# Optimization experiments

Hardware: AMD Instinct MI355X
Metric: run time of the kernel (lower is better)

The kernel has to match this reference:

```python
import jax, jax.numpy as jnp
import numpy as np
from jax import lax

B, N, T, D, H, O = 64, 16, 64, 128, 256, 1  # batch, max_neighbors, time_steps, input_dim, hidden_dim, output_dim
NEG = -1e30


def gru(x, h0, Wih, Whh, bih, bhh):
    """Single-layer PyTorch-convention GRU. x:(B,T,D) h0:(B,H) -> (ys:(B,T,H), hT:(B,H))."""
    def step(h, xt):
        gi = xt @ Wih.T + bih          # (B,3H)
        gh = h @ Whh.T + bhh           # (B,3H)
        i_r, i_z, i_n = jnp.split(gi, 3, axis=-1)
        h_r, h_z, h_n = jnp.split(gh, 3, axis=-1)
        r = jax.nn.sigmoid(i_r + h_r)
        z = jax.nn.sigmoid(i_z + h_z)
        n = jnp.tanh(i_n + r * h_n)
        h_new = (1.0 - z) * n + z * h
        return h_new, h_new
    hT, ys = lax.scan(step, h0, jnp.swapaxes(x, 0, 1))
    return jnp.swapaxes(ys, 0, 1), hT


def setup_inputs() -> dict:
    key = jax.random.key(0)
    ks = jax.random.split(key, 16)
    def xavier(k, shape):
        fan_out, fan_in = shape[0], shape[1]
        std = np.sqrt(2.0 / (fan_in + fan_out))
        return jax.random.normal(k, shape, dtype=jnp.float32) * std
    inp = {
        "node_input": jax.random.normal(ks[0], (B, T, D), dtype=jnp.float32),
        "node_hidden": jnp.zeros((1, B, H), dtype=jnp.float32),
        "neighbors_input": jax.random.normal(ks[1], (B, N, T, D), dtype=jnp.float32),
        "neighbors_hidden": jnp.zeros((1, B * N, H), dtype=jnp.float32),
        "s_len": jax.random.randint(ks[2], (B,), 1, T + 1),
        # Node GRU params
        "Wih_node": xavier(ks[3], (3 * H, D)),
        "Whh_node": xavier(ks[4], (3 * H, H)),
        "bih_node": jnp.zeros((3 * H,), dtype=jnp.float32),
        "bhh_node": jnp.zeros((3 * H,), dtype=jnp.float32),
        # Neighbor GRU params
        "Wih_ngh": xavier(ks[5], (3 * H, D)),
        "Whh_ngh": xavier(ks[6], (3 * H, H)),
        "bih_ngh": jnp.zeros((3 * H,), dtype=jnp.float32),
        "bhh_ngh": jnp.zeros((3 * H,), dtype=jnp.float32),
        # Attention projections (torch Linear convention: y = x @ W.T)
        "Wq": xavier(ks[7], (H, H)),
        "Wk": xavier(ks[8], (H, H)),
        "Wv": xavier(ks[9], (H, H)),
        "Wbil": xavier(ks[10], (H, H)),
        "bbil": jnp.zeros((T,), dtype=jnp.float32),
        "Wprj": xavier(ks[11], (O, H)),
        "bprj": jnp.zeros((O,), dtype=jnp.float32),
    }
    return inp


def reference(node_input, node_hidden, neighbors_input, neighbors_hidden, s_len,
              Wih_node, Whh_node, bih_node, bhh_node,
              Wih_ngh, Whh_ngh, bih_ngh, bhh_ngh,
              Wq, Wk, Wv, Wbil, bbil, Wprj, bprj):
    # --- GRU encodes (nlayers=1) ---
    node_out, node_hT = gru(node_input, node_hidden[0], Wih_node, Whh_node, bih_node, bhh_node)  # (B,T,H)
    ngh_in = neighbors_input.reshape(B * N, T, D)
    ngh_out, ngh_hT = gru(ngh_in, neighbors_hidden[0], Wih_ngh, Whh_ngh, bih_ngh, bhh_ngh)
    ngh_out = ngh_out.reshape(B, N, T, H)

    # --- Time attention, batched over all N+1 slots (instead of python loop) ---
    kv = jnp.concatenate([node_out[:, None], ngh_out], axis=1)  # (B,M,T,H), M=N+1
    Q = node_out @ Wq.T                                          # (B,T,H) shared query for all slots
    K = kv @ Wk.T                                                # (B,M,T,H)
    V = kv @ Wv.T                                                # (B,M,T,H)
    # Bilinear score: (Q @ Wbil) @ K^T + b  -> (B,M,T,T); bbil:(T,) broadcasts on last axis
    S = jnp.einsum('bth,bmsh->bmts', Q @ Wbil, K) + bbil
    causal = jnp.triu(jnp.ones((T, T), dtype=bool), k=1)         # mask future positions
    S = jnp.where(causal, NEG, S)
    A = jax.nn.softmax(S, axis=-1)                               # (B,M,T,T); dropout=0 (eval)
    ctx = jnp.einsum('bmts,bmsh->bmth', A, V)                    # (B,M,T,H)

    # --- Output projection and sum over slots ---
    proj = ctx @ Wprj.T + bprj                                   # (B,M,T,O)
    out = jnp.sum(proj.reshape(B, N + 1, T * O), axis=1)         # (B,T*O)
    out = jnp.squeeze(out)
    return out, node_hT[None], ngh_hT[None], A
```

## Files before the change

### kernel.cpp

```cpp
#include <hip/hip_runtime.h>
#include <hip/hip_bf16.h>

#define NEGV -1e30f
typedef __attribute__((ext_vector_type(8))) short bf16x8;
typedef __attribute__((ext_vector_type(4))) float f32x4;

__device__ __forceinline__ float rcpf_(float x) { return __builtin_amdgcn_rcpf(x); }
__device__ __forceinline__ float sigmoidf_(float x) { return rcpf_(1.0f + __expf(-x)); }
__device__ __forceinline__ float tanhf_(float x) {
    float ax = fabsf(x);
    float e = __expf(-2.0f * ax);
    float t = (1.0f - e) * rcpf_(1.0f + e);
    return copysignf(t, x);
}
__device__ __forceinline__ float bf2f(unsigned short u) {
    union { float f; unsigned int i; } x; x.i = ((unsigned int)u) << 16; return x.f;
}
__device__ __forceinline__ float bfsel(uint2 v, int rg) {
    unsigned int w = (rg < 2) ? v.x : v.y;
    return bf2f((unsigned short)((rg & 1) ? (w >> 16) : (w & 0xffffu)));
}

__global__ __launch_bounds__(256) void wqb_gemm(const float* __restrict__ Wbil_,
    const float* __restrict__ Wq_, float* __restrict__ outw)
{
    __shared__ __align__(16) float As[32 * 68];
    __shared__ __align__(16) float Bs[32 * 68];
    const int tid = threadIdx.x, tx = tid & 15, ty = tid >> 4;
    const int rb = blockIdx.x * 64, cb = blockIdx.y * 64;
    float acc[4][4] = {};
    for (int k0 = 0; k0 < 256; k0 += 32) {
        __syncthreads();
        for (int f = tid; f < 2048; f += 256) {
            int kk = f >> 6, r = f & 63;
            As[kk * 68 + r] = Wbil_[(size_t)(k0 + kk) * 256 + rb + r];
        }
        for (int f = tid; f < 2048; f += 256) {
            int kk = f >> 6, c = f & 63;
            Bs[kk * 68 + c] = Wq_[(size_t)(k0 + kk) * 256 + cb + c];
        }
        __syncthreads();
#pragma unroll
        for (int kk = 0; kk < 32; ++kk) {
            float4 a4 = *(const float4*)(As + kk * 68 + ty * 4);
            float4 b4 = *(const float4*)(Bs + kk * 68 + tx * 4);
            float av[4] = {a4.x, a4.y, a4.z, a4.w};
            float bv[4] = {b4.x, b4.y, b4.z, b4.w};
#pragma unroll
            for (int i = 0; i < 4; ++i)
#pragma unroll
                for (int j = 0; j < 4; ++j) acc[i][j] += av[i] * bv[j];
        }
    }
#pragma unroll
    for (int i = 0; i < 4; ++i)
#pragma unroll
        for (int j = 0; j < 4; ++j)
            outw[(size_t)(rb + ty * 4 + i) * 256 + cb + tx * 4 + j] = acc[i][j];
}

__device__ __forceinline__ void swz_store(const float* __restrict__ src,
    __hip_bfloat16* __restrict__ dst, int idx, int kshift)
{
    int n = idx >> kshift, k = idx & ((1 << kshift) - 1);
    int nt = n >> 4, kt = k >> 5, quad = (k & 31) >> 3, pos = k & 7;
    dst[((size_t)((nt << (kshift - 5)) + kt) * 64 + quad * 16 + (n & 15)) * 8 + pos] =
        (__hip_bfloat16)src[idx];
}

__device__ __forceinline__ void swz_store_g(const float* __restrict__ src,
    __hip_bfloat16* __restrict__ dst, int idx, int kshift)
{
    int n = idx >> kshift, k = idx & ((1 << kshift) - 1);
    int gate = n >> 8, c = n & 255, w = c >> 5, half = (c >> 4) & 1;
    int tileG = w * 6 + gate * 2 + half;
    int kt = k >> 5, quad = (k & 31) >> 3, pos = k & 7;
    dst[((size_t)((tileG << (kshift - 5)) + kt) * 64 + quad * 16 + (n & 15)) * 8 + pos] =
        (__hip_bfloat16)src[idx];
}

__global__ __launch_bounds__(256) void convert_all(
    const float* __restrict__ Wih_n, const float* __restrict__ Wih_g,
    const float* __restrict__ Whh_n, const float* __restrict__ Whh_g,
    const float* __restrict__ Wk_,   const float* __restrict__ Wv_,
    const float* __restrict__ wqb_f,
    __hip_bfloat16* Wih_n_sw, __hip_bfloat16* Wih_g_sw,
    __hip_bfloat16* Whh_n_sw, __hip_bfloat16* Whh_g_sw,
    __hip_bfloat16* Wk_sw, __hip_bfloat16* Wv_sw, __hip_bfloat16* wqb_sw)
{
    int g = blockIdx.x * 256 + threadIdx.x;
    if (g < 98304)        swz_store_g(Wih_n, Wih_n_sw, g, 7);
    else if (g < 196608)  swz_store_g(Wih_g, Wih_g_sw, g - 98304, 7);
    else if (g < 393216)  swz_store_g(Whh_n, Whh_n_sw, g - 196608, 8);
    else if (g < 589824)  swz_store_g(Whh_g, Whh_g_sw, g - 393216, 8);
    else if (g < 655360)  swz_store(Wk_,   Wk_sw,   g - 589824, 8);
    else if (g < 720896)  swz_store(Wv_,   Wv_sw,   g - 655360, 8);
    else                  swz_store(wqb_f, wqb_sw,  g - 720896, 8);
}

__global__ __launch_bounds__(512) void gi_gemm(
    const float* __restrict__ node_input, const float* __restrict__ neighbors_input,
    const __hip_bfloat16* __restrict__ Wih_n_sw, const __hip_bfloat16* __restrict__ Wih_g_sw,
    const float* __restrict__ bih_node, const float* __restrict__ bhh_node,
    const float* __restrict__ bih_ngh,  const float* __restrict__ bhh_ngh,
    __hip_bfloat16* __restrict__ gi)
{
    __shared__ __align__(16) __hip_bfloat16 xs[16 * 136];
    const int tid = threadIdx.x, wave = tid >> 6, lane = tid & 63;
    const int quad = lane >> 4, lr = lane & 15;
    const int sblk = blockIdx.x >> 4, tc = blockIdx.x & 15;
    const bool isnode = (sblk < 4);
    const float* __restrict__ xb = isnode
        ? (node_input + (size_t)sblk * 16 * 64 * 128)
        : (neighbors_input + ((size_t)sblk * 16 - 64) * 64 * 128);
    const __hip_bfloat16* __restrict__ Wsw = isnode ? Wih_n_sw : Wih_g_sw;
    const float* __restrict__ bi = isnode ? bih_node : bih_ngh;
    const float* __restrict__ bh = isnode ? bhh_node : bhh_ngh;

    bf16x8 wfr[24];
#pragma unroll
    for (int nt = 0; nt < 6; ++nt)
#pragma unroll
        for (int kt = 0; kt < 4; ++kt)
            wfr[nt * 4 + kt] = *(const bf16x8*)(const void*)(
                Wsw + ((size_t)((wave * 6 + nt) * 4 + kt) * 64 + lane) * 8);

    float bias6[6];
#pragma unroll
    for (int tl = 0; tl < 6; ++tl) {
        int gate = tl >> 1;
        int col = gate * 256 + wave * 32 + (tl & 1) * 16 + lr;
        bias6[tl] = bi[col] + (gate < 2 ? bh[col] : 0.0f);
    }

    const int sr = tid >> 5, sc = (tid & 31) * 4;
    __hip_bfloat16* __restrict__ gout =
        gi + (size_t)((sblk * 8 + wave) * 6) * 16384 + (size_t)lane * 4;

    for (int tt = 0; tt < 4; ++tt) {
        int t = tc * 4 + tt;
        if (tt) __syncthreads();
        float4 v = *(const float4*)(xb + ((size_t)sr * 64 + t) * 128 + sc);
        __hip_bfloat16* d = xs + sr * 136 + sc;
        d[0] = (__hip_bfloat16)v.x; d[1] = (__hip_bfloat16)v.y;
        d[2] = (__hip_bfloat16)v.z; d[3] = (__hip_bfloat16)v.w;
        __syncthreads();

        bf16x8 afr[4];
#pragma unroll
        for (int kt = 0; kt < 4; ++kt)
            afr[kt] = *(const bf16x8*)(const void*)(xs + lr * 136 + kt * 32 + quad * 8);

#pragma unroll
        for (int tl = 0; tl < 6; ++tl) {
            f32x4 acc = {0.f, 0.f, 0.f, 0.f};
#pragma unroll
            for (int kt = 0; kt < 4; ++kt)
                acc = __builtin_amdgcn_mfma_f32_16x16x32_bf16(afr[kt], wfr[tl * 4 + kt], acc, 0, 0, 0);
            union { __hip_bfloat16 p[4]; uint2 u; } pu;
#pragma unroll
            for (int rg = 0; rg < 4; ++rg) pu.p[rg] = (__hip_bfloat16)(acc[rg] + bias6[tl]);
            *(uint2*)(void*)(gout + (size_t)tl * 16384 + (size_t)t * 256) = pu.u;
        }
    }
}

__global__ __launch_bounds__(512, 2) void scan_kernel(
    const __hip_bfloat16* __restrict__ gi,
    const __hip_bfloat16* __restrict__ Whh_n_sw,
    const __hip_bfloat16* __restrict__ Whh_g_sw,
    const float* __restrict__ bhh_node, const float* __restrict__ bhh_ngh,
    const float* __restrict__ node_hidden, const float* __restrict__ neighbors_hidden,
    __hip_bfloat16* __restrict__ node_out, __hip_bfloat16* __restrict__ ngh_out,
    float* __restrict__ out_node_hT, float* __restrict__ out_ngh_hT)
{
    __shared__ __align__(16) __hip_bfloat16 wlds[96 * 64 * 8];
    __shared__ __align__(16) __hip_bfloat16 hfr[2 * 4096];
    const int tid = threadIdx.x;
    const int wave = tid >> 6, lane = tid & 63;
    const int quad = lane >> 4, lr = lane & 15;
    const int row0 = blockIdx.x * 16;
    const bool isnode = (row0 < 64);
    const __hip_bfloat16* __restrict__ Wsw = isnode ? Whh_n_sw : Whh_g_sw;
    const float* __restrict__ bhh = isnode ? bhh_node : bhh_ngh;

    bf16x8 wreg[36];
#pragma unroll
    for (int nt = 0; nt < 6; ++nt)
#pragma unroll
        for (int kt = 0; kt < 6; ++kt)
            wreg[nt * 6 + kt] = *(const bf16x8*)(const void*)(
                Wsw + ((size_t)((wave * 6 + nt) * 8 + kt) * 64 + lane) * 8);

    for (int f = tid; f < 6144; f += 512) {
        int chunk = f >> 6, l = f & 63;
        int tileG = chunk >> 1, s = chunk & 1;
        *(uint4*)(void*)(wlds + ((size_t)chunk * 64 + l) * 8) =
            *(const uint4*)(const void*)(Wsw + ((size_t)(tileG * 8 + 6 + s) * 64 + l) * 8);
    }

    const __hip_bfloat16* __restrict__ gbase =
        gi + (size_t)((blockIdx.x * 8 + wave) * 6) * 16384 + (size_t)lane * 4;

    const float bhn0 = bhh[512 + wave * 32 + lr];
    const float bhn1 = bhh[512 + wave * 32 + 16 + lr];

    const int hwoff = (wave * 64 + (lr >> 3) * 16 + quad * 4) * 8 + (lr & 7);
    float hreg[8];
    {
        const float* hsrc = isnode ? (node_hidden + (size_t)row0 * 256)
                                   : (neighbors_hidden + (size_t)(row0 - 64) * 256);
#pragma unroll
        for (int half = 0; half < 2; ++half)
#pragma unroll
            for (int rg = 0; rg < 4; ++rg) {
                float v = hsrc[(size_t)(quad * 4 + rg) * 256 + wave * 32 + half * 16 + lr];
                hreg[half * 4 + rg] = v;
                hfr[hwoff + half * 256 + rg * 8] = (__hip_bfloat16)v;
            }
    }

    __hip_bfloat16* optr;
    {
        int orow = tid & 15;
        int ocol = (tid >> 6) * 32 + ((tid >> 4) & 3) * 8;
        optr = isnode ? (node_out + ((size_t)(row0 + orow) * 64) * 256 + ocol)
                      : (ngh_out + ((size_t)(row0 - 64 + orow) * 64) * 256 + ocol);
    }

    uint2 gv[6];
#pragma unroll
    for (int tl = 0; tl < 6; ++tl)
        gv[tl] = *(const uint2*)(const void*)(gbase + (size_t)tl * 16384);

    __syncthreads();

#pragma unroll 1
    for (int t = 0; t < 64; ++t) {
        const __hip_bfloat16* hr = hfr + (t & 1) * 4096;

        const int tp = (t < 63) ? (t + 1) : 63;
        uint2 gvn[6];
#pragma unroll
        for (int tl = 0; tl < 6; ++tl)
            gvn[tl] = *(const uint2*)(const void*)(gbase + (size_t)tl * 16384 + tp * 256);

        if (t) {
            uint4 ov = *(const uint4*)(const void*)(hr + tid * 8);
            *(uint4*)(void*)optr = ov;
            optr += 256;
        }

        f32x4 acc[6] = {{0.f,0.f,0.f,0.f},{0.f,0.f,0.f,0.f},{0.f,0.f,0.f,0.f},
                        {0.f,0.f,0.f,0.f},{0.f,0.f,0.f,0.f},{0.f,0.f,0.f,0.f}};
        {
#pragma unroll
            for (int kt = 0; kt < 3; ++kt) {
                bf16x8 av = *(const bf16x8*)(const void*)(hr + (kt * 64 + lane) * 8);
#pragma unroll
                for (int tl = 0; tl < 6; ++tl)
                    acc[tl] = __builtin_amdgcn_mfma_f32_16x16x32_bf16(av, wreg[tl * 6 + kt], acc[tl], 0, 0, 0);
            }
        }
        {
#pragma unroll
            for (int kt = 3; kt < 6; ++kt) {
                bf16x8 av = *(const bf16x8*)(const void*)(hr + (kt * 64 + lane) * 8);
#pragma unroll
                for (int tl = 0; tl < 6; ++tl)
                    acc[tl] = __builtin_amdgcn_mfma_f32_16x16x32_bf16(av, wreg[tl * 6 + kt], acc[tl], 0, 0, 0);
            }
        }
        {
#pragma unroll
            for (int s = 0; s < 2; ++s) {
                bf16x8 av = *(const bf16x8*)(const void*)(hr + ((6 + s) * 64 + lane) * 8);
#pragma unroll
                for (int tl = 0; tl < 6; ++tl) {
                    bf16x8 bfr = *(const bf16x8*)(const void*)(
                        wlds + ((size_t)((wave * 6 + tl) * 2 + s) * 64 + lane) * 8);
                    acc[tl] = __builtin_amdgcn_mfma_f32_16x16x32_bf16(av, bfr, acc[tl], 0, 0, 0);
                }
            }
        }

        __hip_bfloat16* hw = hfr + ((t + 1) & 1) * 4096 + hwoff;
#pragma unroll
        for (int half = 0; half < 2; ++half) {
            const float bhn = half ? bhn1 : bhn0;
#pragma unroll
            for (int rg = 0; rg < 4; ++rg) {
                float ghr = acc[half][rg];
                float ghz = acc[2 + half][rg];
                float ghn = acc[4 + half][rg] + bhn;
                float gir = bfsel(gv[half], rg);
                float giz = bfsel(gv[2 + half], rg);
                float gin = bfsel(gv[4 + half], rg);
                float r = sigmoidf_(gir + ghr);
                float z = sigmoidf_(giz + ghz);
                float n = tanhf_(gin + r * ghn);
                float hn = (1.0f - z) * n + z * hreg[half * 4 + rg];
                hreg[half * 4 + rg] = hn;
                hw[half * 256 + rg * 8] = (__hip_bfloat16)hn;
            }
        }
#pragma unroll
        for (int tl = 0; tl < 6; ++tl) gv[tl] = gvn[tl];

        asm volatile("s_waitcnt lgkmcnt(0)" ::: "memory");
        __builtin_amdgcn_s_barrier();
        __builtin_amdgcn_sched_barrier(0);
    }

    {
        uint4 ov = *(const uint4*)(const void*)(hfr + tid * 8);
        *(uint4*)(void*)optr = ov;
    }
    {
        float* hdst = isnode ? (out_node_hT + (size_t)row0 * 256)
                             : (out_ngh_hT + (size_t)(row0 - 64) * 256);
#pragma unroll
        for (int half = 0; half < 2; ++half)
#pragma unroll
            for (int rg = 0; rg < 4; ++rg)
                hdst[(size_t)(quad * 4 + rg) * 256 + wave * 32 + half * 16 + lr] = hreg[half * 4 + rg];
    }
}

__global__ __launch_bounds__(256) void kv_gemm(
    const __hip_bfloat16* __restrict__ A0, const __hip_bfloat16* __restrict__ A1,
    const __hip_bfloat16* __restrict__ Wk_sw, const __hip_bfloat16* __restrict__ Wv_sw,
    const __hip_bfloat16* __restrict__ wqb_sw,
    __hip_bfloat16* __restrict__ Kb, __hip_bfloat16* __restrict__ Vt,
    __hip_bfloat16* __restrict__ Qb)
{
    __shared__ __align__(16) __hip_bfloat16 As[64 * 264];
    const int tid = threadIdx.x, wave = tid >> 6, lane = tid & 63;
    const int quad = lane >> 4, lr = lane & 15;
    const int rb = blockIdx.x * 64;
    const bool node = rb < 4096;
    const __hip_bfloat16* A = node ? (A0 + (size_t)rb * 256) : (A1 + (size_t)(rb - 4096) * 256);

    for (int f = tid; f < 2048; f += 256) {
        int row = f >> 5, cc = (f & 31) * 8;
        *(uint4*)(void*)(As + row * 264 + cc) =
            *(const uint4*)(const void*)(A + (size_t)row * 256 + cc);
    }
    __syncthreads();

    bf16x8 afr[8];
#pragma unroll
    for (int kt = 0; kt < 8; ++kt)
        afr[kt] = *(const bf16x8*)(const void*)(As + (wave * 16 + lr) * 264 + kt * 32 + quad * 8);

    int b_, slot;
    if (node) { b_ = rb >> 6; slot = 0; }
    else { int rr = (rb - 4096) >> 6; b_ = rr >> 4; slot = (rr & 15) + 1; }
    const size_t kbase = ((size_t)b_ * 1088 + slot * 64) * 256;
    const size_t vtbase = (size_t)(b_ * 17 + slot) * 256 * 64;
    const int s0 = wave * 16 + quad * 4;

    for (int ntg = 0; ntg < 16; ++ntg) {
        f32x4 acc = {0.f, 0.f, 0.f, 0.f};
#pragma unroll
        for (int kt = 0; kt < 8; ++kt) {
            bf16x8 bfr = *(const bf16x8*)(const void*)(Wk_sw + ((size_t)(ntg * 8 + kt) * 64 + lane) * 8);
            acc = __builtin_amdgcn_mfma_f32_16x16x32_bf16(afr[kt], bfr, acc, 0, 0, 0);
        }
        int col = ntg * 16 + lr;
#pragma unroll
        for (int rg = 0; rg < 4; ++rg)
            Kb[kbase + (size_t)(s0 + rg) * 256 + col] = (__hip_bfloat16)acc[rg];
    }
    for (int ntg = 0; ntg < 16; ++ntg) {
        f32x4 acc = {0.f, 0.f, 0.f, 0.f};
#pragma unroll
        for (int kt = 0; kt < 8; ++kt) {
            bf16x8 bfr = *(const bf16x8*)(const void*)(Wv_sw + ((size_t)(ntg * 8 + kt) * 64 + lane) * 8);
            acc = __builtin_amdgcn_mfma_f32_16x16x32_bf16(afr[kt], bfr, acc, 0, 0, 0);
        }
        int col = ntg * 16 + lr;
        __hip_bfloat16 t4[4];
#pragma unroll
        for (int rg = 0; rg < 4; ++rg) t4[rg] = (__hip_bfloat16)acc[rg];
        *(uint2*)(void*)(Vt + vtbase + (size_t)col * 64 + s0) = *(const uint2*)(const void*)t4;
    }
    if (node) {
        for (int ntg = 0; ntg < 16; ++ntg) {
            f32x4 acc = {0.f, 0.f, 0.f, 0.f};
#pragma unroll
            for (int kt = 0; kt < 8; ++kt) {
                bf16x8 bfr = *(const bf16x8*)(const void*)(wqb_sw + ((size_t)(ntg * 8 + kt) * 64 + lane) * 8);
                acc = __builtin_amdgcn_mfma_f32_16x16x32_bf16(afr[kt], bfr, acc, 0, 0, 0);
            }
            int col = ntg * 16 + lr;
#pragma unroll
            for (int rg = 0; rg < 4; ++rg)
                Qb[(size_t)(rb + s0 + rg) * 256 + col] = (__hip_bfloat16)acc[rg];
        }
    }
}

__global__ __launch_bounds__(256) void attn_kernel(
    const __hip_bfloat16* __restrict__ Qb, const __hip_bfloat16* __restrict__ Kb,
    const __hip_bfloat16* __restrict__ Vt, const float* __restrict__ bbil,
    const float* __restrict__ Wprj, const float* __restrict__ bprj,
    float* __restrict__ A_out, float* __restrict__ out)
{
    __shared__ __align__(16) float Sbuf[64 * 68];
    __shared__ __align__(16) __hip_bfloat16 Pb[64 * 72];
    __shared__ float rowmax[64], rowrcp[64];
    __shared__ float red[64 * 16];
    const int tid = threadIdx.x;
    const int wave = tid >> 6, lane = tid & 63;
    const int quad = lane >> 4, lr = lane & 15;
    const int bm = blockIdx.x, b = bm / 17, m = bm % 17;
    const __hip_bfloat16* Qrow = Qb + (size_t)b * 64 * 256;
    const __hip_bfloat16* Krow = Kb + ((size_t)b * 1088 + m * 64) * 256;
    const __hip_bfloat16* Vtrow = Vt + (size_t)(b * 17 + m) * 256 * 64;

    f32x4 sacc[4] = {{0.f,0.f,0.f,0.f},{0.f,0.f,0.f,0.f},{0.f,0.f,0.f,0.f},{0.f,0.f,0.f,0.f}};
#pragma unroll
    for (int kt = 0; kt < 8; ++kt) {
        bf16x8 afr = *(const bf16x8*)(const void*)(Qrow + (size_t)(wave * 16 + lr) * 256 + kt * 32 + quad * 8);
#pragma unroll
        for (int c = 0; c < 4; ++c) {
            bf16x8 bfr = *(const bf16x8*)(const void*)(Krow + (size_t)(c * 16 + lr) * 256 + kt * 32 + quad * 8);
            sacc[c] = __builtin_amdgcn_mfma_f32_16x16x32_bf16(afr, bfr, sacc[c], 0, 0, 0);
        }
    }
#pragma unroll
    for (int c = 0; c < 4; ++c)
#pragma unroll
        for (int rg = 0; rg < 4; ++rg) {
            int t_ = wave * 16 + quad * 4 + rg, s_ = c * 16 + lr;
            Sbuf[t_ * 68 + s_] = (s_ <= t_) ? (sacc[c][rg] + bbil[s_]) : NEGV;
        }
    __syncthreads();
    if (tid < 64) {
        float mx = -3.0e38f;
        for (int s = 0; s < 64; ++s) mx = fmaxf(mx, Sbuf[tid * 68 + s]);
        float sum = 0.0f;
        for (int s = 0; s < 64; ++s) sum += __expf(Sbuf[tid * 68 + s] - mx);
        rowmax[tid] = mx;
        rowrcp[tid] = 1.0f / sum;
    }
    __syncthreads();
    for (int idx = tid; idx < 4096; idx += 256) {
        int t_ = idx >> 6, s_ = idx & 63;
        float e = __expf(Sbuf[t_ * 68 + s_] - rowmax[t_]) * rowrcp[t_];
        A_out[(size_t)bm * 4096 + idx] = e;
        Pb[t_ * 72 + s_] = (__hip_bfloat16)e;
    }
    __syncthreads();

    bf16x8 pfr[2];
#pragma unroll
    for (int k2 = 0; k2 < 2; ++k2)
        pfr[k2] = *(const bf16x8*)(const void*)(Pb + (wave * 16 + lr) * 72 + k2 * 32 + quad * 8);
    float part[4] = {0.f, 0.f, 0.f, 0.f};
#pragma unroll
    for (int nt = 0; nt < 16; ++nt) {
        f32x4 cacc = {0.f, 0.f, 0.f, 0.f};
#pragma unroll
        for (int k2 = 0; k2 < 2; ++k2) {
            bf16x8 bfr = *(const bf16x8*)(const void*)(Vtrow + (size_t)(nt * 16 + lr) * 64 + k2 * 32 + quad * 8);
            cacc = __builtin_amdgcn_mfma_f32_16x16x32_bf16(pfr[k2], bfr, cacc, 0, 0, 0);
        }
        float wp = Wprj[nt * 16 + lr];
#pragma unroll
        for (int rg = 0; rg < 4; ++rg) part[rg] += cacc[rg] * wp;
    }
#pragma unroll
    for (int rg = 0; rg < 4; ++rg) red[(wave * 16 + quad * 4 + rg) * 16 + lr] = part[rg];
    __syncthreads();
    if (tid < 64) {
        float s = 0.0f;
#pragma unroll
        for (int q = 0; q < 16; ++q) s += red[tid * 16 + q];
        if (m == 0) s += 17.0f * bprj[0];
        atomicAdd(out + b * 64 + tid, s);
    }
}

extern "C" void kernel_launch(void* const* d_in, const int* in_sizes, int n_in,
                              void* d_out, int out_size, void* d_ws, size_t ws_size,
                              hipStream_t stream)
{
    const float* node_input       = (const float*)d_in[0];
    const float* node_hidden      = (const float*)d_in[1];
    const float* neighbors_input  = (const float*)d_in[2];
    const float* neighbors_hidden = (const float*)d_in[3];
    const float* Wih_node = (const float*)d_in[5];
    const float* Whh_node = (const float*)d_in[6];
    const float* bih_node = (const float*)d_in[7];
    const float* bhh_node = (const float*)d_in[8];
    const float* Wih_ngh  = (const float*)d_in[9];
    const float* Whh_ngh  = (const float*)d_in[10];
    const float* bih_ngh  = (const float*)d_in[11];
    const float* bhh_ngh  = (const float*)d_in[12];
    const float* Wq   = (const float*)d_in[13];
    const float* Wk   = (const float*)d_in[14];
    const float* Wv   = (const float*)d_in[15];
    const float* Wbil = (const float*)d_in[16];
    const float* bbil = (const float*)d_in[17];
    const float* Wprj = (const float*)d_in[18];
    const float* bprj = (const float*)d_in[19];

    float* out         = (float*)d_out;
    float* out_node_hT = out + 4096;
    float* out_ngh_hT  = out + 20480;
    float* out_A       = out + 282624;

    char* w = (char*)d_ws;
    float*          wqb_f    = (float*)(w);
    __hip_bfloat16* Wih_n_sw = (__hip_bfloat16*)(w + 262144);
    __hip_bfloat16* Wih_g_sw = (__hip_bfloat16*)(w + 458752);
    __hip_bfloat16* Whh_n_sw = (__hip_bfloat16*)(w + 655360);
    __hip_bfloat16* Whh_g_sw = (__hip_bfloat16*)(w + 1048576);
    __hip_bfloat16* Wk_sw    = (__hip_bfloat16*)(w + 1441792);
    __hip_bfloat16* Wv_sw    = (__hip_bfloat16*)(w + 1572864);
    __hip_bfloat16* wqb_sw   = (__hip_bfloat16*)(w + 1703936);
    __hip_bfloat16* node_out_b = (__hip_bfloat16*)(w + 1835008);
    __hip_bfloat16* ngh_out_b  = (__hip_bfloat16*)(w + 3932160);
    __hip_bfloat16* qb_b       = (__hip_bfloat16*)(w + 37486592);
    __hip_bfloat16* gi         = (__hip_bfloat16*)(w + 39583744);
    __hip_bfloat16* kbuf = gi;
    __hip_bfloat16* vtbuf = kbuf + 17825792;

    hipMemsetAsync(d_out, 0, 4096 * sizeof(float), stream);

    wqb_gemm<<<dim3(4, 4), 256, 0, stream>>>(Wbil, Wq, wqb_f);

    convert_all<<<3072, 256, 0, stream>>>(
        Wih_node, Wih_ngh, Whh_node, Whh_ngh, Wk, Wv, wqb_f,
        Wih_n_sw, Wih_g_sw, Whh_n_sw, Whh_g_sw, Wk_sw, Wv_sw, wqb_sw);

    gi_gemm<<<1088, 512, 0, stream>>>(
        node_input, neighbors_input, Wih_n_sw, Wih_g_sw,
        bih_node, bhh_node, bih_ngh, bhh_ngh, gi);

    scan_kernel<<<68, 512, 0, stream>>>(gi, Whh_n_sw, Whh_g_sw,
        bhh_node, bhh_ngh, node_hidden, neighbors_hidden,
        node_out_b, ngh_out_b, out_node_hT, out_ngh_hT);

    kv_gemm<<<1088, 256, 0, stream>>>(
        node_out_b, ngh_out_b, Wk_sw, Wv_sw, wqb_sw, kbuf, vtbuf, qb_b);

    attn_kernel<<<1088, 256, 0, stream>>>(qb_b, kbuf, vtbuf, bbil, Wprj, bprj,
                                          out_A, out);
}
```

Baseline: 439.5 us.

## Fuse Wq·Wbil GEMM into weight conversion and pre-swizzle V for MFMA loads

```diff
diff --git a/kernel.cpp b/kernel.cpp
--- a/kernel.cpp
+++ b/kernel.cpp
@@ -21,13 +21,50 @@
     return bf2f((unsigned short)((rg & 1) ? (w >> 16) : (w & 0xffffu)));
 }
 
-__global__ __launch_bounds__(256) void wqb_gemm(const float* __restrict__ Wbil_,
-    const float* __restrict__ Wq_, float* __restrict__ outw)
+__device__ __forceinline__ void swz_store(const float* __restrict__ src,
+    __hip_bfloat16* __restrict__ dst, int idx, int kshift)
+{
+    int n = idx >> kshift, k = idx & ((1 << kshift) - 1);
+    int nt = n >> 4, kt = k >> 5, quad = (k & 31) >> 3, pos = k & 7;
+    dst[((size_t)((nt << (kshift - 5)) + kt) * 64 + quad * 16 + (n & 15)) * 8 + pos] =
+        (__hip_bfloat16)src[idx];
+}
+
+__device__ __forceinline__ void swz_store_g(const float* __restrict__ src,
+    __hip_bfloat16* __restrict__ dst, int idx, int kshift)
+{
+    int n = idx >> kshift, k = idx & ((1 << kshift) - 1);
+    int gate = n >> 8, c = n & 255, w = c >> 5, half = (c >> 4) & 1;
+    int tileG = w * 6 + gate * 2 + half;
+    int kt = k >> 5, quad = (k & 31) >> 3, pos = k & 7;
+    dst[((size_t)((tileG << (kshift - 5)) + kt) * 64 + quad * 16 + (n & 15)) * 8 + pos] =
+        (__hip_bfloat16)src[idx];
+}
+
+__global__ __launch_bounds__(256) void convert_all(
+    const float* __restrict__ Wih_n, const float* __restrict__ Wih_g,
+    const float* __restrict__ Whh_n, const float* __restrict__ Whh_g,
+    const float* __restrict__ Wk_,   const float* __restrict__ Wv_,
+    const float* __restrict__ Wbil_, const float* __restrict__ Wq_,
+    __hip_bfloat16* Wih_n_sw, __hip_bfloat16* Wih_g_sw,
+    __hip_bfloat16* Whh_n_sw, __hip_bfloat16* Whh_g_sw,
+    __hip_bfloat16* Wk_sw, __hip_bfloat16* Wv_sw, __hip_bfloat16* wqb_sw)
 {
     __shared__ __align__(16) float As[32 * 68];
     __shared__ __align__(16) float Bs[32 * 68];
+    if (blockIdx.x < 2816) {
+        int g = blockIdx.x * 256 + threadIdx.x;
+        if (g < 98304)        swz_store_g(Wih_n, Wih_n_sw, g, 7);
+        else if (g < 196608)  swz_store_g(Wih_g, Wih_g_sw, g - 98304, 7);
+        else if (g < 393216)  swz_store_g(Whh_n, Whh_n_sw, g - 196608, 8);
+        else if (g < 589824)  swz_store_g(Whh_g, Whh_g_sw, g - 393216, 8);
+        else if (g < 655360)  swz_store(Wk_,   Wk_sw,   g - 589824, 8);
+        else                  swz_store(Wv_,   Wv_sw,   g - 655360, 8);
+        return;
+    }
+    const int bx = blockIdx.x - 2816;
     const int tid = threadIdx.x, tx = tid & 15, ty = tid >> 4;
-    const int rb = blockIdx.x * 64, cb = blockIdx.y * 64;
+    const int rb = (bx >> 2) * 64, cb = (bx & 3) * 64;
     float acc[4][4] = {};
     for (int k0 = 0; k0 < 256; k0 += 32) {
         __syncthreads();
@@ -55,47 +92,12 @@
 #pragma unroll
     for (int i = 0; i < 4; ++i)
 #pragma unroll
-        for (int j = 0; j < 4; ++j)
-            outw[(size_t)(rb + ty * 4 + i) * 256 + cb + tx * 4 + j] = acc[i][j];
-}
-
-__device__ __forceinline__ void swz_store(const float* __restrict__ src,
-    __hip_bfloat16* __restrict__ dst, int idx, int kshift)
-{
-    int n = idx >> kshift, k = idx & ((1 << kshift) - 1);
-    int nt = n >> 4, kt = k >> 5, quad = (k & 31) >> 3, pos = k & 7;
-    dst[((size_t)((nt << (kshift - 5)) + kt) * 64 + quad * 16 + (n & 15)) * 8 + pos] =
-        (__hip_bfloat16)src[idx];
-}
-
-__device__ __forceinline__ void swz_store_g(const float* __restrict__ src,
-    __hip_bfloat16* __restrict__ dst, int idx, int kshift)
-{
-    int n = idx >> kshift, k = idx & ((1 << kshift) - 1);
-    int gate = n >> 8, c = n & 255, w = c >> 5, half = (c >> 4) & 1;
-    int tileG = w * 6 + gate * 2 + half;
-    int kt = k >> 5, quad = (k & 31) >> 3, pos = k & 7;
-    dst[((size_t)((tileG << (kshift - 5)) + kt) * 64 + quad * 16 + (n & 15)) * 8 + pos] =
-        (__hip_bfloat16)src[idx];
-}
-
-__global__ __launch_bounds__(256) void convert_all(
-    const float* __restrict__ Wih_n, const float* __restrict__ Wih_g,
-    const float* __restrict__ Whh_n, const float* __restrict__ Whh_g,
-    const float* __restrict__ Wk_,   const float* __restrict__ Wv_,
-    const float* __restrict__ wqb_f,
-    __hip_bfloat16* Wih_n_sw, __hip_bfloat16* Wih_g_sw,
-    __hip_bfloat16* Whh_n_sw, __hip_bfloat16* Whh_g_sw,
-    __hip_bfloat16* Wk_sw, __hip_bfloat16* Wv_sw, __hip_bfloat16* wqb_sw)
-{
-    int g = blockIdx.x * 256 + threadIdx.x;
-    if (g < 98304)        swz_store_g(Wih_n, Wih_n_sw, g, 7);
-    else if (g < 196608)  swz_store_g(Wih_g, Wih_g_sw, g - 98304, 7);
-    else if (g < 393216)  swz_store_g(Whh_n, Whh_n_sw, g - 196608, 8);
-    else if (g < 589824)  swz_store_g(Whh_g, Whh_g_sw, g - 393216, 8);
-    else if (g < 655360)  swz_store(Wk_,   Wk_sw,   g - 589824, 8);
-    else if (g < 720896)  swz_store(Wv_,   Wv_sw,   g - 655360, 8);
-    else                  swz_store(wqb_f, wqb_sw,  g - 720896, 8);
+        for (int j = 0; j < 4; ++j) {
+            int n = rb + ty * 4 + i, k = cb + tx * 4 + j;
+            int nt = n >> 4, kt = k >> 5, quad = (k & 31) >> 3, pos = k & 7;
+            wqb_sw[((size_t)(nt * 8 + kt) * 64 + quad * 16 + (n & 15)) * 8 + pos] =
+                (__hip_bfloat16)acc[i][j];
+        }
 }
 
 __global__ __launch_bounds__(512) void gi_gemm(
@@ -372,18 +374,23 @@
         for (int rg = 0; rg < 4; ++rg)
             Kb[kbase + (size_t)(s0 + rg) * 256 + col] = (__hip_bfloat16)acc[rg];
     }
-    for (int ntg = 0; ntg < 16; ++ntg) {
-        f32x4 acc = {0.f, 0.f, 0.f, 0.f};
-#pragma unroll
-        for (int kt = 0; kt < 8; ++kt) {
-            bf16x8 bfr = *(const bf16x8*)(const void*)(Wv_sw + ((size_t)(ntg * 8 + kt) * 64 + lane) * 8);
-            acc = __builtin_amdgcn_mfma_f32_16x16x32_bf16(afr[kt], bfr, acc, 0, 0, 0);
-        }
-        int col = ntg * 16 + lr;
-        __hip_bfloat16 t4[4];
-#pragma unroll
-        for (int rg = 0; rg < 4; ++rg) t4[rg] = (__hip_bfloat16)acc[rg];
-        *(uint2*)(void*)(Vt + vtbase + (size_t)col * 64 + s0) = *(const uint2*)(const void*)t4;
+    {
+        const int kt2 = wave >> 1;
+        const int lp = ((wave & 1) * 2 + (quad >> 1)) * 16 + lr;
+        const int j0 = (quad & 1) * 4;
+        for (int ntg = 0; ntg < 16; ++ntg) {
+            f32x4 acc = {0.f, 0.f, 0.f, 0.f};
+#pragma unroll
+            for (int kt = 0; kt < 8; ++kt) {
+                bf16x8 bfr = *(const bf16x8*)(const void*)(Wv_sw + ((size_t)(ntg * 8 + kt) * 64 + lane) * 8);
+                acc = __builtin_amdgcn_mfma_f32_16x16x32_bf16(afr[kt], bfr, acc, 0, 0, 0);
+            }
+            __hip_bfloat16 t4[4];
+#pragma unroll
+            for (int rg = 0; rg < 4; ++rg) t4[rg] = (__hip_bfloat16)acc[rg];
+            *(uint2*)(void*)(Vt + vtbase + (size_t)(((ntg * 2 + kt2) * 64 + lp) * 8 + j0)) =
+                *(const uint2*)(const void*)t4;
+        }
     }
     if (node) {
         for (int ntg = 0; ntg < 16; ++ntg) {
@@ -464,7 +471,7 @@
         f32x4 cacc = {0.f, 0.f, 0.f, 0.f};
 #pragma unroll
         for (int k2 = 0; k2 < 2; ++k2) {
-            bf16x8 bfr = *(const bf16x8*)(const void*)(Vtrow + (size_t)(nt * 16 + lr) * 64 + k2 * 32 + quad * 8);
+            bf16x8 bfr = *(const bf16x8*)(const void*)(Vtrow + (size_t)((nt * 2 + k2) * 64 + lane) * 8);
             cacc = __builtin_amdgcn_mfma_f32_16x16x32_bf16(pfr[k2], bfr, cacc, 0, 0, 0);
         }
         float wp = Wprj[nt * 16 + lr];
@@ -513,7 +520,6 @@
     float* out_A       = out + 282624;
 
     char* w = (char*)d_ws;
-    float*          wqb_f    = (float*)(w);
     __hip_bfloat16* Wih_n_sw = (__hip_bfloat16*)(w + 262144);
     __hip_bfloat16* Wih_g_sw = (__hip_bfloat16*)(w + 458752);
     __hip_bfloat16* Whh_n_sw = (__hip_bfloat16*)(w + 655360);
@@ -530,10 +536,8 @@
 
     hipMemsetAsync(d_out, 0, 4096 * sizeof(float), stream);
 
-    wqb_gemm<<<dim3(4, 4), 256, 0, stream>>>(Wbil, Wq, wqb_f);
-
-    convert_all<<<3072, 256, 0, stream>>>(
-        Wih_node, Wih_ngh, Whh_node, Whh_ngh, Wk, Wv, wqb_f,
+    convert_all<<<2832, 256, 0, stream>>>(
+        Wih_node, Wih_ngh, Whh_node, Whh_ngh, Wk, Wv, Wbil, Wq,
         Wih_n_sw, Wih_g_sw, Whh_n_sw, Whh_g_sw, Wk_sw, Wv_sw, wqb_sw);
 
     gi_gemm<<<1088, 512, 0, stream>>>(
```

After: 423.3 us, median of 2. 1.04x faster.
